# Kernel tuning notes

Hardware: AMD Instinct MI355X
Metric: run time of the kernel (lower is better)

The kernel has to match this reference:

```python
import jax, jax.numpy as jnp
import numpy as np

B, N, M, C, G = 8, 1024, 20000, 80, 64
NMS_THR = 0.5
PULL_W = 1.0
PUSH_W = 1.0
EPS = 1e-6


def _rand_boxes(key, shape):
    k1, k2 = jax.random.split(key)
    xy = jax.random.uniform(k1, shape + (2,), minval=0.0, maxval=900.0)
    wh = jax.random.uniform(k2, shape + (2,), minval=8.0, maxval=120.0)
    return jnp.concatenate([xy, xy + wh], axis=-1).astype(jnp.float32)


def setup_inputs() -> dict:
    key = jax.random.key(0)
    ks = jax.random.split(key, 6)
    return {
        "pos_inds": jax.random.randint(ks[0], (B, N), 0, M, dtype=jnp.int32),
        "pos_gt_index": jax.random.randint(ks[1], (B, N), 0, G, dtype=jnp.int32),
        "gt_bboxes": _rand_boxes(ks[2], (B, G)),
        "bbox_preds": _rand_boxes(ks[3], (B, N)),
        "cls_scores": jax.random.uniform(ks[4], (B, M, C), dtype=jnp.float32),
        "gt_labels": jax.random.randint(ks[5], (B, G), 0, C, dtype=jnp.int32),
    }


def pairwise_iou(b1, b2):
    # legacy +1 convention, matching bbox_overlaps(mode='iou')
    lt = jnp.maximum(b1[:, None, :2], b2[None, :, :2])
    rb = jnp.minimum(b1[:, None, 2:], b2[None, :, 2:])
    wh = jnp.clip(rb - lt + 1.0, 0.0)
    ov = wh[..., 0] * wh[..., 1]
    a1 = (b1[:, 2] - b1[:, 0] + 1.0) * (b1[:, 3] - b1[:, 1] + 1.0)
    a2 = (b2[:, 2] - b2[:, 0] + 1.0) * (b2[:, 3] - b2[:, 1] + 1.0)
    return ov / (a1[:, None] + a2[None, :] - ov)


def nms_loss_single(boxes, scores, gt_index, gt_boxes):
    # boxes [N,4], scores [N], gt_index [N] int, gt_boxes [G,4]
    n = boxes.shape[0]
    g_n = gt_boxes.shape[0]
    # push_select=True: first operand of IoU is detached
    iou = pairwise_iou(jax.lax.stop_gradient(boxes), boxes)  # [N,N]
    gtiou = jax.lax.stop_gradient(pairwise_iou(gt_boxes, gt_boxes))  # [G,G]
    s_det = jax.lax.stop_gradient(scores)

    init = (jnp.ones((n,), bool), -jnp.ones((g_n,), jnp.int32),
            jnp.float32(0.0), jnp.float32(0.0), jnp.int32(0), jnp.int32(0))

    def step(carry, _):
        alive, seen, tpull, tpush, pcnt, qcnt = carry
        any_alive = jnp.any(alive)
        i = jnp.argmax(jnp.where(alive, s_det, -jnp.inf))  # pop highest score
        g = gt_index[i]
        prev = seen[g]
        has_seen = (prev >= 0) & any_alive
        # pull: pull_relax=True, use_score=True
        max_s_iou = jnp.maximum(iou[prev, i], EPS)
        pull = jnp.where(has_seen, -jnp.log(1.0 - NMS_THR + max_s_iou) * scores[i], 0.0)
        seen = jnp.where(any_alive & (prev < 0), seen.at[g].set(i.astype(jnp.int32)), seen)
        pcnt = pcnt + has_seen.astype(jnp.int32)
        alive = alive.at[i].set(False)
        remaining = jnp.any(alive)  # torch breaks (dropping this step's pull) if empty
        row = iou[i]
        overlap = alive & (row > NMS_THR)
        push_mask = overlap & (gt_index != g) & (row > gtiou[g, gt_index])
        n_push = jnp.sum(push_mask)
        # push: push_relax=False, use_score=True, scores NOT detached
        terms = -jnp.log(jnp.where(push_mask, 1.0 - row, 1.0)) * scores
        push = jnp.where(n_push > 0,
                         jnp.sum(jnp.where(push_mask, terms, 0.0)) / jnp.maximum(n_push, 1).astype(jnp.float32),
                         0.0)
        add = any_alive & remaining
        tpull = tpull + jnp.where(add, pull, 0.0)
        tpush = tpush + jnp.where(add, push, 0.0)
        qcnt = qcnt + jnp.where(add, n_push.astype(jnp.int32), 0)
        alive = alive & ~overlap
        return (alive, seen, tpull, tpush, pcnt, qcnt), None

    (alive, seen, tpull, tpush, pcnt, qcnt), _ = jax.lax.scan(step, init, None, length=n)
    pull = tpull / (pcnt.astype(jnp.float32) + EPS)
    push = tpush / (qcnt.astype(jnp.float32) + EPS)
    return push, pull


def reference(pos_inds, pos_gt_index, gt_bboxes, bbox_preds, cls_scores, gt_labels):
    labels = jnp.take_along_axis(gt_labels, pos_gt_index, axis=1)            # [B,N]
    sel = jnp.take_along_axis(cls_scores, pos_inds[..., None], axis=1)       # [B,N,C]
    scores = jnp.take_along_axis(sel, labels[..., None].astype(jnp.int32), axis=2)[..., 0]  # [B,N]
    push, pull = jax.vmap(nms_loss_single)(bbox_preds, scores, pos_gt_index, gt_bboxes)
    return jnp.stack([jnp.mean(push) * PUSH_W, jnp.mean(pull) * PULL_W])
```

## Files before the change

kernel.cpp:

```cpp
#include <hip/hip_runtime.h>
#include <math.h>

#define B_ 8
#define N_ 1024
#define M_ 20000
#define C_ 80
#define G_ 64
typedef unsigned long long ull;

#define WS_BOX_OFF  0
#define WS_META_OFF 131072
#define WS_ADJ_OFF  262144

__device__ __forceinline__ float iou1(float ax, float ay, float az, float aw,
                                      float bx, float by, float bz, float bw) {
    float lx = fmaxf(ax, bx), ly = fmaxf(ay, by);
    float rx = fminf(az, bz), ry = fminf(aw, bw);
    float w = fmaxf(rx - lx + 1.0f, 0.0f), h = fmaxf(ry - ly + 1.0f, 0.0f);
    float ov = w * h;
    float a1 = (az - ax + 1.0f) * (aw - ay + 1.0f);
    float a2 = (bz - bx + 1.0f) * (bw - by + 1.0f);
    return ov / (a1 + a2 - ov);
}

__global__ __launch_bounds__(1024) void prep_kernel(
    const int* __restrict__ pos_inds, const int* __restrict__ pos_gt,
    const float* __restrict__ bbox_preds, const float* __restrict__ cls_scores,
    const int* __restrict__ gt_labels, float4* __restrict__ boxesG,
    float2* __restrict__ metaG, float* __restrict__ out) {
    const int b = blockIdx.x, t = threadIdx.x;
    __shared__ ull s_k2[2][N_];

    if (b == 0 && t == 0) { out[0] = 0.f; out[1] = 0.f; }

    int g0 = pos_gt[b * N_ + t];
    int lab = gt_labels[b * G_ + g0];
    int pi = pos_inds[b * N_ + t];
    float s = cls_scores[(size_t)b * (M_ * C_) + (size_t)pi * C_ + lab];
    ull key = ((ull)(~__float_as_uint(s)) << 32) | (unsigned)t;

    int pb = 0;
    for (unsigned k2 = 2; k2 <= N_; k2 <<= 1) {
        for (unsigned jj = k2 >> 1; jj; jj >>= 1) {
            ull other;
            if (jj >= 64) {
                s_k2[pb][t] = key;
                __syncthreads();
                other = s_k2[pb][t ^ jj];
                pb ^= 1;
            } else {
                int lo = __shfl_xor((int)(unsigned)key, (int)jj);
                int hi = __shfl_xor((int)(unsigned)(key >> 32), (int)jj);
                other = ((ull)(unsigned)hi << 32) | (unsigned)lo;
            }
            bool keep_min = (((t & jj) == 0) == ((t & k2) == 0));
            ull mn = key < other ? key : other;
            ull mx = key < other ? other : key;
            key = keep_min ? mn : mx;
        }
    }

    int j = (int)(unsigned)(key & 0xFFFFFFFFull);
    float ss = __uint_as_float(~(unsigned)(key >> 32));
    const float* bp = bbox_preds + (size_t)(b * N_ + j) * 4;
    float x0 = bp[0], y0 = bp[1], x1 = bp[2], y1 = bp[3];
    int g = pos_gt[b * N_ + j];
    boxesG[b * N_ + t] = make_float4(x0, y0, x1, y1);
    metaG[b * N_ + t] = make_float2(__int_as_float(g), ss);
}

__global__ __launch_bounds__(256) void adj_kernel(
    const float4* __restrict__ boxesG, ull* __restrict__ adjG) {
    const int b = blockIdx.y;
    const int r = blockIdx.x * 4 + (threadIdx.x >> 6);
    const int lane = threadIdx.x & 63;
    const int wtop = r >> 6;
    const float4* bb = boxesG + (size_t)b * N_;
    float4 rA = bb[r];
    float ax0 = rA.x, ay0 = rA.y;
    float az1 = rA.z + 1.0f, aw1 = rA.w + 1.0f;
    float a1 = (rA.z - rA.x + 1.0f) * (rA.w - rA.y + 1.0f);
    ull myword = 0ull;
    for (int u = 0; u <= wtop; ++u) {
        float4 cA = bb[u * 64 + lane];
        float lx = fmaxf(ax0, cA.x), ly = fmaxf(ay0, cA.y);
        float rx = fminf(az1, cA.z + 1.0f), ry = fminf(aw1, cA.w + 1.0f);
        float w = fmaxf(rx - lx, 0.0f), h = fmaxf(ry - ly, 0.0f);
        float I = w * h;
        float a2 = (cA.z - cA.x + 1.0f) * (cA.w - cA.y + 1.0f);
        ull word = __ballot(3.0f * I > a1 + a2);
        if (lane == u) myword = word;
    }
    if (lane <= wtop) adjG[(size_t)(b * N_ + r) * 16 + lane] = myword;
}

__global__ __launch_bounds__(1024) void sweep_loss_kernel(
    const float4* __restrict__ boxesG, const float2* __restrict__ metaG,
    const ull* __restrict__ adjG, const float* __restrict__ gt_bboxes,
    float* __restrict__ out) {
    const int b = blockIdx.x, t = threadIdx.x;
    const int wtop = t >> 6, lane = t & 63;

    __shared__ float4 s_box[N_];
    __shared__ float s_score[N_];
    __shared__ short s_g[N_];
    __shared__ float4 s_gt[G_];
    __shared__ ull s_S[16];
    __shared__ unsigned short s_step[N_];
    __shared__ unsigned short s_surv[N_];
    __shared__ float s_ts[N_];
    __shared__ int s_cnt[N_], s_kills[N_], s_first[G_];
    __shared__ int s_wpre[17];
    __shared__ float s_tpull, s_tpush;
    __shared__ int s_pcnt, s_qcnt;

    {
        float4 bx = boxesG[b * N_ + t];
        float2 mt = metaG[b * N_ + t];
        s_box[t] = bx; s_score[t] = mt.y; s_g[t] = (short)__float_as_int(mt.x);
    }
    if (t < G_) s_gt[t] = ((const float4*)gt_bboxes)[b * G_ + t];
    s_ts[t] = 0.f; s_cnt[t] = 0; s_kills[t] = 0; s_step[t] = 0xffff;
    if (t < 16) s_S[t] = 0ull;
    if (t < G_) s_first[t] = 0x7fffffff;
    if (t == 0) { s_tpull = 0.f; s_tpush = 0.f; s_pcnt = 0; s_qcnt = 0; }

    const ull* rowp = adjG + (size_t)(b * N_ + t) * 16;
    ull rw[16];
#pragma unroll
    for (int c = 0; c < 16; ++c) rw[c] = (c <= wtop) ? rowp[c] : 0ull;

    __syncthreads();

    bool alive_f = true;
#pragma unroll
    for (int c = 0; c < 16; ++c) {
        if (wtop == c) {
            ull alive = __ballot(alive_f);
            ull Sc = 0ull;
            const ull below = (1ull << lane) - 1ull;
            const ull myearly = rw[c] & below;
            while (alive) {
                bool me = (alive >> lane) & 1ull;
                bool inU = me && ((myearly & alive) == 0ull);
                ull U = __ballot(inU);
                Sc |= U;
                alive = __ballot(me && !inU && ((myearly & U) == 0ull));
            }
            if (lane == 0) s_S[c] = Sc;
        }
        __syncthreads();
        if (wtop > c && alive_f && (rw[c] & s_S[c]) != 0ull) alive_f = false;
    }

    if (t < 16) s_wpre[t + 1] = __popcll(s_S[t]);
    __syncthreads();
    if (t == 0) { s_wpre[0] = 0; for (int w = 0; w < 16; ++w) s_wpre[w + 1] += s_wpre[w]; }
    __syncthreads();
    const int K = s_wpre[16];
    const ull sbit = 1ull << lane;
    const bool isS = (s_S[wtop] & sbit) != 0ull;
    int myrank = -1;
    if (isS) {
        myrank = s_wpre[wtop] + __popcll(s_S[wtop] & (sbit - 1ull));
        s_step[t] = (unsigned short)myrank;
        s_surv[myrank] = (unsigned short)t;
        atomicMin(&s_first[(int)s_g[t]], myrank);
    }
    __syncthreads();

    if (!isS) {
        int kp = -1;
#pragma unroll
        for (int w = 15; w >= 0; --w) {
            ull m = rw[w] & s_S[w];
            if (w == wtop) m &= (1ull << lane) - 1ull;
            if (m) kp = (w << 6) + (int)(__ffsll(m) - 1);
        }
        if (kp >= 0) {
            int q = s_step[kp];
            atomicAdd(&s_kills[q], 1);
            int gq = (int)s_g[kp], gj = (int)s_g[t];
            if (gq != gj) {
                float4 qa = s_box[kp], ja = s_box[t];
                float ov = iou1(qa.x, qa.y, qa.z, qa.w, ja.x, ja.y, ja.z, ja.w);
                float4 gq4 = s_gt[gq], gj4 = s_gt[gj];
                float gov = iou1(gq4.x, gq4.y, gq4.z, gq4.w,
                                 gj4.x, gj4.y, gj4.z, gj4.w);
                if (ov > gov) {
                    atomicAdd(&s_cnt[q], 1);
                    atomicAdd(&s_ts[q], -__logf(1.0f - ov) * s_score[t]);
                }
            }
        }
    }
    __syncthreads();

    if (isS) {
        int k = myrank, g = (int)s_g[t], f = s_first[g];
        if (f < k) {
            atomicAdd(&s_pcnt, 1);
            bool drop = (k == K - 1) && (s_kills[k] == 0);
            if (!drop) {
                float4 fA = s_box[s_surv[f]], kA = s_box[t];
                float ov = iou1(fA.x, fA.y, fA.z, fA.w, kA.x, kA.y, kA.z, kA.w);
                atomicAdd(&s_tpull, -__logf(0.5f + fmaxf(ov, 1e-6f)) * s_score[t]);
            }
        }
        if (s_cnt[k] > 0) {
            atomicAdd(&s_tpush, s_ts[k] / (float)s_cnt[k]);
            atomicAdd(&s_qcnt, s_cnt[k]);
        }
    }
    __syncthreads();

    if (t == 0) {
        atomicAdd(&out[0], (s_tpush / ((float)s_qcnt + 1e-6f)) * 0.125f);
        atomicAdd(&out[1], (s_tpull / ((float)s_pcnt + 1e-6f)) * 0.125f);
    }
}

extern "C" void kernel_launch(void* const* d_in, const int* in_sizes, int n_in,
                              void* d_out, int out_size, void* d_ws, size_t ws_size,
                              hipStream_t stream) {
    const int* pos_inds = (const int*)d_in[0];
    const int* pos_gt = (const int*)d_in[1];
    const float* gt_bboxes = (const float*)d_in[2];
    const float* bbox_preds = (const float*)d_in[3];
    const float* cls_scores = (const float*)d_in[4];
    const int* gt_labels = (const int*)d_in[5];
    float* out = (float*)d_out;

    float4* boxesG = (float4*)((char*)d_ws + WS_BOX_OFF);
    float2* metaG = (float2*)((char*)d_ws + WS_META_OFF);
    ull* adjG = (ull*)((char*)d_ws + WS_ADJ_OFF);

    prep_kernel<<<dim3(B_), dim3(1024), 0, stream>>>(
        pos_inds, pos_gt, bbox_preds, cls_scores, gt_labels, boxesG, metaG, out);
    adj_kernel<<<dim3(256, B_), dim3(256), 0, stream>>>(boxesG, adjG);
    sweep_loss_kernel<<<dim3(B_), dim3(1024), 0, stream>>>(boxesG, metaG, adjG, gt_bboxes, out);
}
```

Before: 125.3 us.

## Replace per-chunk block barriers with flag-based wavefront chaining in greedy sweep

The sequential 16-chunk greedy NMS resolution used to issue 16 block-wide __syncthreads. It now chains wavefronts through a shared flag, so each wavefront spin-waits only for its predecessors' survivor masks and then resolves its own chunk. It also keeps a single counter for the last survivor instead of a per-survivor kill array, and reduces the pull/push sums with wavefront shuffles before one atomic per wavefront. Spin-waiting on shared memory relies on wavefront forward-progress and memory-ordering behaviour, which risks deadlock or stale reads.

```diff
diff --git a/kernel.cpp b/kernel.cpp
--- a/kernel.cpp
+++ b/kernel.cpp
@@ -109,8 +109,10 @@
     __shared__ unsigned short s_step[N_];
     __shared__ unsigned short s_surv[N_];
     __shared__ float s_ts[N_];
-    __shared__ int s_cnt[N_], s_kills[N_], s_first[G_];
+    __shared__ int s_cnt[N_], s_first[G_];
     __shared__ int s_wpre[17];
+    __shared__ int s_flag;
+    __shared__ int s_kills_last;
     __shared__ float s_tpull, s_tpush;
     __shared__ int s_pcnt, s_qcnt;
 
@@ -120,10 +122,13 @@
         s_box[t] = bx; s_score[t] = mt.y; s_g[t] = (short)__float_as_int(mt.x);
     }
     if (t < G_) s_gt[t] = ((const float4*)gt_bboxes)[b * G_ + t];
-    s_ts[t] = 0.f; s_cnt[t] = 0; s_kills[t] = 0; s_step[t] = 0xffff;
+    s_ts[t] = 0.f; s_cnt[t] = 0; s_step[t] = 0xffff;
     if (t < 16) s_S[t] = 0ull;
     if (t < G_) s_first[t] = 0x7fffffff;
-    if (t == 0) { s_tpull = 0.f; s_tpush = 0.f; s_pcnt = 0; s_qcnt = 0; }
+    if (t == 0) {
+        s_tpull = 0.f; s_tpush = 0.f; s_pcnt = 0; s_qcnt = 0;
+        s_flag = 0; s_kills_last = 0;
+    }
 
     const ull* rowp = adjG + (size_t)(b * N_ + t) * 16;
     ull rw[16];
@@ -132,26 +137,30 @@
 
     __syncthreads();
 
-    bool alive_f = true;
-#pragma unroll
-    for (int c = 0; c < 16; ++c) {
-        if (wtop == c) {
-            ull alive = __ballot(alive_f);
-            ull Sc = 0ull;
-            const ull below = (1ull << lane) - 1ull;
-            const ull myearly = rw[c] & below;
-            while (alive) {
-                bool me = (alive >> lane) & 1ull;
-                bool inU = me && ((myearly & alive) == 0ull);
-                ull U = __ballot(inU);
-                Sc |= U;
-                alive = __ballot(me && !inU && ((myearly & U) == 0ull));
-            }
-            if (lane == 0) s_S[c] = Sc;
-        }
-        __syncthreads();
-        if (wtop > c && alive_f && (rw[c] & s_S[c]) != 0ull) alive_f = false;
-    }
+    {
+        ull dead = 0ull;
+        for (int c = 0; c < wtop; ++c) {
+            while (*((volatile int*)&s_flag) <= c) { }
+            dead |= rw[c] & *((volatile ull*)&s_S[c]);
+        }
+        ull alive = __ballot(dead == 0ull);
+        ull Sc = 0ull;
+        const ull below = (1ull << lane) - 1ull;
+        const ull myearly = rw[wtop] & below;
+        while (alive) {
+            bool me = (alive >> lane) & 1ull;
+            bool inU = me && ((myearly & alive) == 0ull);
+            ull U = __ballot(inU);
+            Sc |= U;
+            alive = __ballot(me && !inU && ((myearly & U) == 0ull));
+        }
+        if (lane == 0) {
+            s_S[wtop] = Sc;
+            __threadfence_block();
+            *((volatile int*)&s_flag) = wtop + 1;
+        }
+    }
+    __syncthreads();
 
     if (t < 16) s_wpre[t + 1] = __popcll(s_S[t]);
     __syncthreads();
@@ -179,7 +188,7 @@
         }
         if (kp >= 0) {
             int q = s_step[kp];
-            atomicAdd(&s_kills[q], 1);
+            if (q == K - 1) atomicAdd(&s_kills_last, 1);
             int gq = (int)s_g[kp], gj = (int)s_g[t];
             if (gq != gj) {
                 float4 qa = s_box[kp], ja = s_box[t];
@@ -196,21 +205,37 @@
     }
     __syncthreads();
 
+    float my_pull = 0.f, my_push = 0.f;
+    int my_p = 0, my_q = 0;
     if (isS) {
         int k = myrank, g = (int)s_g[t], f = s_first[g];
         if (f < k) {
-            atomicAdd(&s_pcnt, 1);
-            bool drop = (k == K - 1) && (s_kills[k] == 0);
+            my_p = 1;
+            bool drop = (k == K - 1) && (s_kills_last == 0);
             if (!drop) {
                 float4 fA = s_box[s_surv[f]], kA = s_box[t];
                 float ov = iou1(fA.x, fA.y, fA.z, fA.w, kA.x, kA.y, kA.z, kA.w);
-                atomicAdd(&s_tpull, -__logf(0.5f + fmaxf(ov, 1e-6f)) * s_score[t]);
+                my_pull = -__logf(0.5f + fmaxf(ov, 1e-6f)) * s_score[t];
             }
         }
-        if (s_cnt[k] > 0) {
-            atomicAdd(&s_tpush, s_ts[k] / (float)s_cnt[k]);
-            atomicAdd(&s_qcnt, s_cnt[k]);
-        }
+        int c = s_cnt[k];
+        if (c > 0) {
+            my_push = s_ts[k] / (float)c;
+            my_q = c;
+        }
+    }
+#pragma unroll
+    for (int off = 32; off; off >>= 1) {
+        my_pull += __shfl_xor(my_pull, off);
+        my_push += __shfl_xor(my_push, off);
+        my_p    += __shfl_xor(my_p, off);
+        my_q    += __shfl_xor(my_q, off);
+    }
+    if (lane == 0) {
+        atomicAdd(&s_tpull, my_pull);
+        atomicAdd(&s_tpush, my_push);
+        atomicAdd(&s_pcnt, my_p);
+        atomicAdd(&s_qcnt, my_q);
     }
     __syncthreads();
 
```

After: 126.7 us. No clear change (+1.1%).
